# Kernel tuning notes

Measured on AMD Instinct MI355X. Metric: run time of the kernel, lower is better.

The kernel has to match this reference:

```python
import jax, jax.numpy as jnp
import numpy as np

B, IN_CAPS, IN_DIM = 64, 512, 128
NUM_CAPS, DIM_CAPS, NUM_ROUTING = 32, 32, 3


def squash(x, axis=-1):
    sn = jnp.sum(x * x, axis=axis, keepdims=True)
    return (sn / (1.0 + sn)) * x / (jnp.sqrt(sn) + 1e-8)


def setup_inputs() -> dict:
    key = jax.random.key(0)
    k1, k2, k3 = jax.random.split(key, 3)
    input_tensor = jax.random.normal(k1, (B, IN_CAPS, IN_DIM), dtype=jnp.float32)
    W = 0.001 * jax.random.normal(k2, (NUM_CAPS, IN_DIM, DIM_CAPS), dtype=jnp.float32)
    b0 = jax.random.uniform(k3, (B, NUM_CAPS, IN_CAPS, 1), dtype=jnp.float32)
    return {"input_tensor": input_tensor, "W": W, "b0": b0}


def reference(input_tensor, W, b0):
    # u_hat: (B, num_caps, in_caps, dim_caps)
    u_hat = jnp.einsum('bid,ndc->bnic', input_tensor, W)
    temp_u_hat = jax.lax.stop_gradient(u_hat)
    b = b0
    for _ in range(NUM_ROUTING - 1):
        c = jax.nn.softmax(b, axis=1)            # (B, num_caps, in_caps, 1)
        s = jnp.sum(c * temp_u_hat, axis=2)      # (B, num_caps, dim_caps)
        v = squash(s)
        uv = jnp.einsum('bnic,bnc->bni', temp_u_hat, v)[..., None]
        b = b + uv
    c = jax.nn.softmax(b, axis=1)
    s = jnp.sum(c * u_hat, axis=2)
    return squash(s)                             # (B, num_caps, dim_caps)
```

## Files before the change

kernel.cpp:

```cpp
#include <hip/hip_runtime.h>
#include <math.h>

#define Bsz 64
#define IC  512
#define KD  128
#define NC  32
#define DC  32
#define CHUNK 64
#define NCH   8
#define NBLK  512
#define NTHR  256

#define CSTR 36

#define CXP_SZ (Bsz * NCH * NC * KD)
#define WV_SZ  (Bsz * NC * KD)
#define BB_SZ  (Bsz * NC * IC)

__device__ __forceinline__ int xaddr(int i, int kq) {
    return i * KD + ((((kq) + (i >> 2)) & 31) << 2);
}

__global__ __launch_bounds__(NTHR)
void kA(const float* __restrict__ bb_in, const float* __restrict__ x_g,
        float* __restrict__ cxp)
{
    __shared__ float x_s[CHUNK * KD];
    __shared__ float bb_s[NC][CHUNK];
    __shared__ float c_sT[CHUNK * CSTR];

    const int t = threadIdx.x, blk = blockIdx.x;
    const int b = blk >> 3, ch = blk & 7, i0g = ch * CHUNK;

    for (int rep = 0; rep < 8; ++rep) {
        int v = t + rep * NTHR;
        int i = v >> 5, kq = v & 31;
        float4 val = *(const float4*)(x_g + ((size_t)(b * IC + i0g + i)) * KD + (kq << 2));
        *(float4*)(x_s + xaddr(i, kq)) = val;
    }
    for (int rep = 0; rep < 2; ++rep) {
        int v = t + rep * NTHR;
        int n = v >> 4, i4 = v & 15;
        *(float4*)(&bb_s[n][i4 << 2]) =
            *(const float4*)(bb_in + ((size_t)(b * NC + n)) * IC + i0g + (i4 << 2));
    }
    __syncthreads();

    if (t < CHUNK) {
        const int ii = t;
        float m = -1e30f;
        #pragma unroll
        for (int n = 0; n < NC; ++n) m = fmaxf(m, bb_s[n][ii]);
        float e[NC]; float sum = 0.f;
        #pragma unroll
        for (int n = 0; n < NC; ++n) { float ev = __expf(bb_s[n][ii] - m); e[n] = ev; sum += ev; }
        const float inv = 1.f / sum;
        float* crow = c_sT + ii * CSTR;
        #pragma unroll
        for (int n = 0; n < NC; ++n) crow[n] = e[n] * inv;
    }
    __syncthreads();

    const int tn = t & 7, tk = t >> 3;
    const int n0 = tn << 2;
    float4 acc0 = {0,0,0,0}, acc1 = {0,0,0,0}, acc2 = {0,0,0,0}, acc3 = {0,0,0,0};
    for (int ii = 0; ii < CHUNK; ++ii) {
        const float4 c4 = *(const float4*)(c_sT + ii * CSTR + n0);
        const float4 x4 = *(const float4*)(x_s + xaddr(ii, tk));
        acc0.x += c4.x*x4.x; acc0.y += c4.x*x4.y; acc0.z += c4.x*x4.z; acc0.w += c4.x*x4.w;
        acc1.x += c4.y*x4.x; acc1.y += c4.y*x4.y; acc1.z += c4.y*x4.z; acc1.w += c4.y*x4.w;
        acc2.x += c4.z*x4.x; acc2.y += c4.z*x4.y; acc2.z += c4.z*x4.z; acc2.w += c4.z*x4.w;
        acc3.x += c4.w*x4.x; acc3.y += c4.w*x4.y; acc3.z += c4.w*x4.z; acc3.w += c4.w*x4.w;
    }
    float* base = cxp + ((size_t)(b * NCH + ch)) * NC * KD + (tk << 2);
    *(float4*)(base + (size_t)(n0 + 0) * KD) = acc0;
    *(float4*)(base + (size_t)(n0 + 1) * KD) = acc1;
    *(float4*)(base + (size_t)(n0 + 2) * KD) = acc2;
    *(float4*)(base + (size_t)(n0 + 3) * KD) = acc3;
}

__global__ __launch_bounds__(NTHR)
void kB(const float* __restrict__ cxp, const float* __restrict__ W_g,
        float* __restrict__ wv_g, float* __restrict__ out_g, int final_)
{
    __shared__ float w_s[KD * DC];
    __shared__ float cxs[4 * KD];
    __shared__ float vs_s[4][DC];

    const int t = threadIdx.x, blk = blockIdx.x;
    const int pb_n = blk & 31, pb_b0 = (blk >> 5) * 4;

    for (int rep = 0; rep < 4; ++rep) {
        int v = t + rep * NTHR;
        *(float4*)(w_s + (v << 2)) = *(const float4*)(W_g + (size_t)pb_n * KD * DC + (v << 2));
    }
    if (t < 128) {
        const int bsub = t >> 5, k4 = t & 31;
        float4 s4 = {0,0,0,0};
        const float* p = cxp + (((size_t)(pb_b0 + bsub) * NCH) * NC + pb_n) * KD + (k4 << 2);
        #pragma unroll
        for (int c2 = 0; c2 < NCH; ++c2) {
            float4 v4 = *(const float4*)(p + (size_t)c2 * NC * KD);
            s4.x += v4.x; s4.y += v4.y; s4.z += v4.z; s4.w += v4.w;
        }
        *(float4*)(cxs + bsub * KD + (k4 << 2)) = s4;
    }
    __syncthreads();

    if (t < 128) {
        const int bsub = t >> 5, d = t & 31;
        float s = 0.f;
        const float* crow = cxs + bsub * KD;
        for (int k = 0; k < KD; ++k) s += crow[k] * w_s[k * DC + d];
        float sn = s * s;
        #pragma unroll
        for (int off = 1; off < 32; off <<= 1) sn += __shfl_xor(sn, off, 64);
        const float vv = s * (sn / ((1.f + sn) * (sqrtf(sn) + 1e-8f)));
        if (final_) {
            out_g[((size_t)(pb_b0 + bsub) * NC + pb_n) * DC + d] = vv;
        } else {
            vs_s[bsub][d] = vv;
        }
    }
    if (!final_) {
        __syncthreads();
        const int bsub = t >> 6, kk = t & 63;
        for (int k = kk; k < KD; k += 64) {
            float acc = 0.f;
            const float* wrow = w_s + k * DC;
            const float* vrow = &vs_s[bsub][0];
            #pragma unroll
            for (int d = 0; d < DC; ++d) acc += wrow[d] * vrow[d];
            wv_g[((size_t)(pb_b0 + bsub) * NC + pb_n) * KD + k] = acc;
        }
    }
}

__global__ __launch_bounds__(NTHR)
void kC(const float* __restrict__ bb_in, const float* __restrict__ x_g,
        const float* __restrict__ wv_g, float* __restrict__ bb_out)
{
    __shared__ float x_s[CHUNK * KD];
    __shared__ float bb_s[NC][CHUNK];
    __shared__ float wv_sT[KD * CSTR];

    const int t = threadIdx.x, blk = blockIdx.x;
    const int b = blk >> 3, ch = blk & 7, i0g = ch * CHUNK;

    for (int rep = 0; rep < 8; ++rep) {
        int v = t + rep * NTHR;
        int i = v >> 5, kq = v & 31;
        float4 val = *(const float4*)(x_g + ((size_t)(b * IC + i0g + i)) * KD + (kq << 2));
        *(float4*)(x_s + xaddr(i, kq)) = val;
    }
    for (int rep = 0; rep < 2; ++rep) {
        int v = t + rep * NTHR;
        int n = v >> 4, i4 = v & 15;
        *(float4*)(&bb_s[n][i4 << 2]) =
            *(const float4*)(bb_in + ((size_t)(b * NC + n)) * IC + i0g + (i4 << 2));
    }
    for (int rep = 0; rep < 4; ++rep) {
        const int n = t & 31;
        const int k4 = (t >> 5) + (rep << 3);
        float4 v4 = *(const float4*)(wv_g + ((size_t)(b * NC) + n) * KD + (k4 << 2));
        wv_sT[(k4 * 4 + 0) * CSTR + n] = v4.x;
        wv_sT[(k4 * 4 + 1) * CSTR + n] = v4.y;
        wv_sT[(k4 * 4 + 2) * CSTR + n] = v4.z;
        wv_sT[(k4 * 4 + 3) * CSTR + n] = v4.w;
    }
    __syncthreads();

    if (t < 128) {
        const int tn = t & 7, ti = t >> 3;
        const int n0 = tn << 2, i0 = ti << 2;
        float4 a0 = {0,0,0,0}, a1 = {0,0,0,0}, a2 = {0,0,0,0}, a3 = {0,0,0,0};
        for (int kq = 0; kq < 32; ++kq) {
            const float4 xr0 = *(const float4*)(x_s + xaddr(i0 + 0, kq));
            const float4 xr1 = *(const float4*)(x_s + xaddr(i0 + 1, kq));
            const float4 xr2 = *(const float4*)(x_s + xaddr(i0 + 2, kq));
            const float4 xr3 = *(const float4*)(x_s + xaddr(i0 + 3, kq));
            const float4 w0 = *(const float4*)(wv_sT + (kq * 4 + 0) * CSTR + n0);
            const float4 w1 = *(const float4*)(wv_sT + (kq * 4 + 1) * CSTR + n0);
            const float4 w2 = *(const float4*)(wv_sT + (kq * 4 + 2) * CSTR + n0);
            const float4 w3 = *(const float4*)(wv_sT + (kq * 4 + 3) * CSTR + n0);
            a0.x += xr0.x*w0.x + xr0.y*w1.x + xr0.z*w2.x + xr0.w*w3.x;
            a0.y += xr0.x*w0.y + xr0.y*w1.y + xr0.z*w2.y + xr0.w*w3.y;
            a0.z += xr0.x*w0.z + xr0.y*w1.z + xr0.z*w2.z + xr0.w*w3.z;
            a0.w += xr0.x*w0.w + xr0.y*w1.w + xr0.z*w2.w + xr0.w*w3.w;
            a1.x += xr1.x*w0.x + xr1.y*w1.x + xr1.z*w2.x + xr1.w*w3.x;
            a1.y += xr1.x*w0.y + xr1.y*w1.y + xr1.z*w2.y + xr1.w*w3.y;
            a1.z += xr1.x*w0.z + xr1.y*w1.z + xr1.z*w2.z + xr1.w*w3.z;
            a1.w += xr1.x*w0.w + xr1.y*w1.w + xr1.z*w2.w + xr1.w*w3.w;
            a2.x += xr2.x*w0.x + xr2.y*w1.x + xr2.z*w2.x + xr2.w*w3.x;
            a2.y += xr2.x*w0.y + xr2.y*w1.y + xr2.z*w2.y + xr2.w*w3.y;
            a2.z += xr2.x*w0.z + xr2.y*w1.z + xr2.z*w2.z + xr2.w*w3.z;
            a2.w += xr2.x*w0.w + xr2.y*w1.w + xr2.z*w2.w + xr2.w*w3.w;
            a3.x += xr3.x*w0.x + xr3.y*w1.x + xr3.z*w2.x + xr3.w*w3.x;
            a3.y += xr3.x*w0.y + xr3.y*w1.y + xr3.z*w2.y + xr3.w*w3.y;
            a3.z += xr3.x*w0.z + xr3.y*w1.z + xr3.z*w2.z + xr3.w*w3.z;
            a3.w += xr3.x*w0.w + xr3.y*w1.w + xr3.z*w2.w + xr3.w*w3.w;
        }
        bb_s[n0+0][i0+0] += a0.x; bb_s[n0+1][i0+0] += a0.y; bb_s[n0+2][i0+0] += a0.z; bb_s[n0+3][i0+0] += a0.w;
        bb_s[n0+0][i0+1] += a1.x; bb_s[n0+1][i0+1] += a1.y; bb_s[n0+2][i0+1] += a1.z; bb_s[n0+3][i0+1] += a1.w;
        bb_s[n0+0][i0+2] += a2.x; bb_s[n0+1][i0+2] += a2.y; bb_s[n0+2][i0+2] += a2.z; bb_s[n0+3][i0+2] += a2.w;
        bb_s[n0+0][i0+3] += a3.x; bb_s[n0+1][i0+3] += a3.y; bb_s[n0+2][i0+3] += a3.z; bb_s[n0+3][i0+3] += a3.w;
    }
    __syncthreads();

    for (int rep = 0; rep < 2; ++rep) {
        int v = t + rep * NTHR;
        int n = v >> 4, i4 = v & 15;
        *(float4*)(bb_out + ((size_t)(b * NC + n)) * IC + i0g + (i4 << 2)) =
            *(const float4*)(&bb_s[n][i4 << 2]);
    }
}

extern "C" void kernel_launch(void* const* d_in, const int* in_sizes, int n_in,
                              void* d_out, int out_size, void* d_ws, size_t ws_size,
                              hipStream_t stream) {
    const float* x  = (const float*)d_in[0];
    const float* W  = (const float*)d_in[1];
    const float* b0 = (const float*)d_in[2];
    float* out = (float*)d_out;

    float* cxp   = (float*)d_ws;
    float* wv    = cxp + CXP_SZ;
    float* bb_ws = wv + WV_SZ;

    kA<<<NBLK, NTHR, 0, stream>>>(b0, x, cxp);
    kB<<<NBLK, NTHR, 0, stream>>>(cxp, W, wv, out, 0);
    kC<<<NBLK, NTHR, 0, stream>>>(b0, x, wv, bb_ws);
    kA<<<NBLK, NTHR, 0, stream>>>(bb_ws, x, cxp);
    kB<<<NBLK, NTHR, 0, stream>>>(cxp, W, wv, out, 0);
    kC<<<NBLK, NTHR, 0, stream>>>(bb_ws, x, wv, bb_ws);
    kA<<<NBLK, NTHR, 0, stream>>>(bb_ws, x, cxp);
    kB<<<NBLK, NTHR, 0, stream>>>(cxp, W, wv, out, 1);
}
```

Measured before the change: 132.5 us.

## Fuse logit update into softmax-weighted reduction kernel and slim projection kernel

The separate kernel that updated the routing logits is merged into the kernel that computes softmax and the weighted sum over input capsules. This drops two launches and an extra read of x and the logits per routing iteration, and the last iteration no longer writes the logits back. The projection kernel now runs with 128 threads, pads the W tile to avoid bank conflicts, and computes the W·v product for four batches per thread. In exchange the fused kernel uses more shared memory per block, and its serial uv phase only uses half the threads.

```diff
diff --git a/kernel.cpp b/kernel.cpp
--- a/kernel.cpp
+++ b/kernel.cpp
@@ -10,24 +10,27 @@
 #define NCH   8
 #define NBLK  512
 #define NTHR  256
+#define NTHRB 128
 
 #define CSTR 36
+#define BSTR 68
+#define WSTR 33
 
 #define CXP_SZ (Bsz * NCH * NC * KD)
 #define WV_SZ  (Bsz * NC * KD)
-#define BB_SZ  (Bsz * NC * IC)
 
 __device__ __forceinline__ int xaddr(int i, int kq) {
     return i * KD + ((((kq) + (i >> 2)) & 31) << 2);
 }
 
 __global__ __launch_bounds__(NTHR)
-void kA(const float* __restrict__ bb_in, const float* __restrict__ x_g,
-        float* __restrict__ cxp)
+void kACX(const float* __restrict__ bb_in, const float* __restrict__ x_g,
+          const float* __restrict__ wv_g, float* __restrict__ bb_out,
+          float* __restrict__ cxp, int do_uv, int write_bb)
 {
     __shared__ float x_s[CHUNK * KD];
-    __shared__ float bb_s[NC][CHUNK];
-    __shared__ float c_sT[CHUNK * CSTR];
+    __shared__ float bb_s[NC * BSTR];
+    __shared__ float scr[KD * CSTR];
 
     const int t = threadIdx.x, blk = blockIdx.x;
     const int b = blk >> 3, ch = blk & 7, i0g = ch * CHUNK;
@@ -35,27 +38,89 @@
     for (int rep = 0; rep < 8; ++rep) {
         int v = t + rep * NTHR;
         int i = v >> 5, kq = v & 31;
-        float4 val = *(const float4*)(x_g + ((size_t)(b * IC + i0g + i)) * KD + (kq << 2));
-        *(float4*)(x_s + xaddr(i, kq)) = val;
+        *(float4*)(x_s + xaddr(i, kq)) =
+            *(const float4*)(x_g + ((size_t)(b * IC + i0g + i)) * KD + (kq << 2));
     }
     for (int rep = 0; rep < 2; ++rep) {
         int v = t + rep * NTHR;
         int n = v >> 4, i4 = v & 15;
-        *(float4*)(&bb_s[n][i4 << 2]) =
+        *(float4*)(bb_s + n * BSTR + (i4 << 2)) =
             *(const float4*)(bb_in + ((size_t)(b * NC + n)) * IC + i0g + (i4 << 2));
     }
+    if (do_uv) {
+        for (int rep = 0; rep < 4; ++rep) {
+            const int n = t & 31;
+            const int k4 = (t >> 5) + (rep << 3);
+            float4 v4 = *(const float4*)(wv_g + ((size_t)(b * NC) + n) * KD + (k4 << 2));
+            scr[(k4 * 4 + 0) * CSTR + n] = v4.x;
+            scr[(k4 * 4 + 1) * CSTR + n] = v4.y;
+            scr[(k4 * 4 + 2) * CSTR + n] = v4.z;
+            scr[(k4 * 4 + 3) * CSTR + n] = v4.w;
+        }
+    }
     __syncthreads();
+
+    if (do_uv) {
+        if (t < 128) {
+            const int tn = t & 7, ti = t >> 3;
+            const int n0 = tn << 2, i0 = ti << 2;
+            float4 a0 = {0,0,0,0}, a1 = {0,0,0,0}, a2 = {0,0,0,0}, a3 = {0,0,0,0};
+            for (int kq = 0; kq < 32; ++kq) {
+                const float4 xr0 = *(const float4*)(x_s + xaddr(i0 + 0, kq));
+                const float4 xr1 = *(const float4*)(x_s + xaddr(i0 + 1, kq));
+                const float4 xr2 = *(const float4*)(x_s + xaddr(i0 + 2, kq));
+                const float4 xr3 = *(const float4*)(x_s + xaddr(i0 + 3, kq));
+                const float4 w0 = *(const float4*)(scr + (kq * 4 + 0) * CSTR + n0);
+                const float4 w1 = *(const float4*)(scr + (kq * 4 + 1) * CSTR + n0);
+                const float4 w2 = *(const float4*)(scr + (kq * 4 + 2) * CSTR + n0);
+                const float4 w3 = *(const float4*)(scr + (kq * 4 + 3) * CSTR + n0);
+                a0.x += xr0.x*w0.x + xr0.y*w1.x + xr0.z*w2.x + xr0.w*w3.x;
+                a0.y += xr0.x*w0.y + xr0.y*w1.y + xr0.z*w2.y + xr0.w*w3.y;
+                a0.z += xr0.x*w0.z + xr0.y*w1.z + xr0.z*w2.z + xr0.w*w3.z;
+                a0.w += xr0.x*w0.w + xr0.y*w1.w + xr0.z*w2.w + xr0.w*w3.w;
+                a1.x += xr1.x*w0.x + xr1.y*w1.x + xr1.z*w2.x + xr1.w*w3.x;
+                a1.y += xr1.x*w0.y + xr1.y*w1.y + xr1.z*w2.y + xr1.w*w3.y;
+                a1.z += xr1.x*w0.z + xr1.y*w1.z + xr1.z*w2.z + xr1.w*w3.z;
+                a1.w += xr1.x*w0.w + xr1.y*w1.w + xr1.z*w2.w + xr1.w*w3.w;
+                a2.x += xr2.x*w0.x + xr2.y*w1.x + xr2.z*w2.x + xr2.w*w3.x;
+                a2.y += xr2.x*w0.y + xr2.y*w1.y + xr2.z*w2.y + xr2.w*w3.y;
+                a2.z += xr2.x*w0.z + xr2.y*w1.z + xr2.z*w2.z + xr2.w*w3.z;
+                a2.w += xr2.x*w0.w + xr2.y*w1.w + xr2.z*w2.w + xr2.w*w3.w;
+                a3.x += xr3.x*w0.x + xr3.y*w1.x + xr3.z*w2.x + xr3.w*w3.x;
+                a3.y += xr3.x*w0.y + xr3.y*w1.y + xr3.z*w2.y + xr3.w*w3.y;
+                a3.z += xr3.x*w0.z + xr3.y*w1.z + xr3.z*w2.z + xr3.w*w3.z;
+                a3.w += xr3.x*w0.w + xr3.y*w1.w + xr3.z*w2.w + xr3.w*w3.w;
+            }
+            bb_s[(n0+0)*BSTR + i0+0] += a0.x; bb_s[(n0+1)*BSTR + i0+0] += a0.y;
+            bb_s[(n0+2)*BSTR + i0+0] += a0.z; bb_s[(n0+3)*BSTR + i0+0] += a0.w;
+            bb_s[(n0+0)*BSTR + i0+1] += a1.x; bb_s[(n0+1)*BSTR + i0+1] += a1.y;
+            bb_s[(n0+2)*BSTR + i0+1] += a1.z; bb_s[(n0+3)*BSTR + i0+1] += a1.w;
+            bb_s[(n0+0)*BSTR + i0+2] += a2.x; bb_s[(n0+1)*BSTR + i0+2] += a2.y;
+            bb_s[(n0+2)*BSTR + i0+2] += a2.z; bb_s[(n0+3)*BSTR + i0+2] += a2.w;
+            bb_s[(n0+0)*BSTR + i0+3] += a3.x; bb_s[(n0+1)*BSTR + i0+3] += a3.y;
+            bb_s[(n0+2)*BSTR + i0+3] += a3.z; bb_s[(n0+3)*BSTR + i0+3] += a3.w;
+        }
+        __syncthreads();
+        if (write_bb) {
+            for (int rep = 0; rep < 2; ++rep) {
+                int v = t + rep * NTHR;
+                int n = v >> 4, i4 = v & 15;
+                *(float4*)(bb_out + ((size_t)(b * NC + n)) * IC + i0g + (i4 << 2)) =
+                    *(const float4*)(bb_s + n * BSTR + (i4 << 2));
+            }
+        }
+    }
 
     if (t < CHUNK) {
         const int ii = t;
         float m = -1e30f;
         #pragma unroll
-        for (int n = 0; n < NC; ++n) m = fmaxf(m, bb_s[n][ii]);
+        for (int n = 0; n < NC; ++n) m = fmaxf(m, bb_s[n * BSTR + ii]);
         float e[NC]; float sum = 0.f;
         #pragma unroll
-        for (int n = 0; n < NC; ++n) { float ev = __expf(bb_s[n][ii] - m); e[n] = ev; sum += ev; }
+        for (int n = 0; n < NC; ++n) { float ev = __expf(bb_s[n * BSTR + ii] - m); e[n] = ev; sum += ev; }
         const float inv = 1.f / sum;
-        float* crow = c_sT + ii * CSTR;
+        float* crow = scr + ii * CSTR;
         #pragma unroll
         for (int n = 0; n < NC; ++n) crow[n] = e[n] * inv;
     }
@@ -65,7 +130,7 @@
     const int n0 = tn << 2;
     float4 acc0 = {0,0,0,0}, acc1 = {0,0,0,0}, acc2 = {0,0,0,0}, acc3 = {0,0,0,0};
     for (int ii = 0; ii < CHUNK; ++ii) {
-        const float4 c4 = *(const float4*)(c_sT + ii * CSTR + n0);
+        const float4 c4 = *(const float4*)(scr + ii * CSTR + n0);
         const float4 x4 = *(const float4*)(x_s + xaddr(ii, tk));
         acc0.x += c4.x*x4.x; acc0.y += c4.x*x4.y; acc0.z += c4.x*x4.z; acc0.w += c4.x*x4.w;
         acc1.x += c4.y*x4.x; acc1.y += c4.y*x4.y; acc1.z += c4.y*x4.z; acc1.w += c4.y*x4.w;
@@ -79,22 +144,25 @@
     *(float4*)(base + (size_t)(n0 + 3) * KD) = acc3;
 }
 
-__global__ __launch_bounds__(NTHR)
+__global__ __launch_bounds__(NTHRB)
 void kB(const float* __restrict__ cxp, const float* __restrict__ W_g,
         float* __restrict__ wv_g, float* __restrict__ out_g, int final_)
 {
-    __shared__ float w_s[KD * DC];
+    __shared__ float w_s[KD * WSTR];
     __shared__ float cxs[4 * KD];
     __shared__ float vs_s[4][DC];
 
     const int t = threadIdx.x, blk = blockIdx.x;
     const int pb_n = blk & 31, pb_b0 = (blk >> 5) * 4;
 
-    for (int rep = 0; rep < 4; ++rep) {
-        int v = t + rep * NTHR;
-        *(float4*)(w_s + (v << 2)) = *(const float4*)(W_g + (size_t)pb_n * KD * DC + (v << 2));
-    }
-    if (t < 128) {
+    for (int rep = 0; rep < 8; ++rep) {
+        int v = t + rep * NTHRB;
+        int k = v >> 3, d0 = (v & 7) << 2;
+        float4 w4 = *(const float4*)(W_g + (size_t)pb_n * KD * DC + (v << 2));
+        float* dst = w_s + k * WSTR + d0;
+        dst[0] = w4.x; dst[1] = w4.y; dst[2] = w4.z; dst[3] = w4.w;
+    }
+    {
         const int bsub = t >> 5, k4 = t & 31;
         float4 s4 = {0,0,0,0};
         const float* p = cxp + (((size_t)(pb_b0 + bsub) * NCH) * NC + pb_n) * KD + (k4 << 2);
@@ -107,111 +175,35 @@
     }
     __syncthreads();
 
-    if (t < 128) {
-        const int bsub = t >> 5, d = t & 31;
-        float s = 0.f;
-        const float* crow = cxs + bsub * KD;
-        for (int k = 0; k < KD; ++k) s += crow[k] * w_s[k * DC + d];
-        float sn = s * s;
-        #pragma unroll
-        for (int off = 1; off < 32; off <<= 1) sn += __shfl_xor(sn, off, 64);
-        const float vv = s * (sn / ((1.f + sn) * (sqrtf(sn) + 1e-8f)));
-        if (final_) {
-            out_g[((size_t)(pb_b0 + bsub) * NC + pb_n) * DC + d] = vv;
-        } else {
-            vs_s[bsub][d] = vv;
-        }
-    }
-    if (!final_) {
+    const int bsub = t >> 5, d = t & 31;
+    float s = 0.f;
+    const float* crow = cxs + bsub * KD;
+    for (int k = 0; k < KD; ++k) s += crow[k] * w_s[k * WSTR + d];
+    float sn = s * s;
+    #pragma unroll
+    for (int off = 1; off < 32; off <<= 1) sn += __shfl_xor(sn, off, 64);
+    const float vv = s * (sn / ((1.f + sn) * (sqrtf(sn) + 1e-8f)));
+
+    if (final_) {
+        out_g[((size_t)(pb_b0 + bsub) * NC + pb_n) * DC + d] = vv;
+    } else {
+        vs_s[bsub][d] = vv;
         __syncthreads();
-        const int bsub = t >> 6, kk = t & 63;
-        for (int k = kk; k < KD; k += 64) {
-            float acc = 0.f;
-            const float* wrow = w_s + k * DC;
-            const float* vrow = &vs_s[bsub][0];
-            #pragma unroll
-            for (int d = 0; d < DC; ++d) acc += wrow[d] * vrow[d];
-            wv_g[((size_t)(pb_b0 + bsub) * NC + pb_n) * KD + k] = acc;
-        }
-    }
-}
-
-__global__ __launch_bounds__(NTHR)
-void kC(const float* __restrict__ bb_in, const float* __restrict__ x_g,
-        const float* __restrict__ wv_g, float* __restrict__ bb_out)
-{
-    __shared__ float x_s[CHUNK * KD];
-    __shared__ float bb_s[NC][CHUNK];
-    __shared__ float wv_sT[KD * CSTR];
-
-    const int t = threadIdx.x, blk = blockIdx.x;
-    const int b = blk >> 3, ch = blk & 7, i0g = ch * CHUNK;
-
-    for (int rep = 0; rep < 8; ++rep) {
-        int v = t + rep * NTHR;
-        int i = v >> 5, kq = v & 31;
-        float4 val = *(const float4*)(x_g + ((size_t)(b * IC + i0g + i)) * KD + (kq << 2));
-        *(float4*)(x_s + xaddr(i, kq)) = val;
-    }
-    for (int rep = 0; rep < 2; ++rep) {
-        int v = t + rep * NTHR;
-        int n = v >> 4, i4 = v & 15;
-        *(float4*)(&bb_s[n][i4 << 2]) =
-            *(const float4*)(bb_in + ((size_t)(b * NC + n)) * IC + i0g + (i4 << 2));
-    }
-    for (int rep = 0; rep < 4; ++rep) {
-        const int n = t & 31;
-        const int k4 = (t >> 5) + (rep << 3);
-        float4 v4 = *(const float4*)(wv_g + ((size_t)(b * NC) + n) * KD + (k4 << 2));
-        wv_sT[(k4 * 4 + 0) * CSTR + n] = v4.x;
-        wv_sT[(k4 * 4 + 1) * CSTR + n] = v4.y;
-        wv_sT[(k4 * 4 + 2) * CSTR + n] = v4.z;
-        wv_sT[(k4 * 4 + 3) * CSTR + n] = v4.w;
-    }
-    __syncthreads();
-
-    if (t < 128) {
-        const int tn = t & 7, ti = t >> 3;
-        const int n0 = tn << 2, i0 = ti << 2;
-        float4 a0 = {0,0,0,0}, a1 = {0,0,0,0}, a2 = {0,0,0,0}, a3 = {0,0,0,0};
-        for (int kq = 0; kq < 32; ++kq) {
-            const float4 xr0 = *(const float4*)(x_s + xaddr(i0 + 0, kq));
-            const float4 xr1 = *(const float4*)(x_s + xaddr(i0 + 1, kq));
-            const float4 xr2 = *(const float4*)(x_s + xaddr(i0 + 2, kq));
-            const float4 xr3 = *(const float4*)(x_s + xaddr(i0 + 3, kq));
-            const float4 w0 = *(const float4*)(wv_sT + (kq * 4 + 0) * CSTR + n0);
-            const float4 w1 = *(const float4*)(wv_sT + (kq * 4 + 1) * CSTR + n0);
-            const float4 w2 = *(const float4*)(wv_sT + (kq * 4 + 2) * CSTR + n0);
-            const float4 w3 = *(const float4*)(wv_sT + (kq * 4 + 3) * CSTR + n0);
-            a0.x += xr0.x*w0.x + xr0.y*w1.x + xr0.z*w2.x + xr0.w*w3.x;
-            a0.y += xr0.x*w0.y + xr0.y*w1.y + xr0.z*w2.y + xr0.w*w3.y;
-            a0.z += xr0.x*w0.z + xr0.y*w1.z + xr0.z*w2.z + xr0.w*w3.z;
-            a0.w += xr0.x*w0.w + xr0.y*w1.w + xr0.z*w2.w + xr0.w*w3.w;
-            a1.x += xr1.x*w0.x + xr1.y*w1.x + xr1.z*w2.x + xr1.w*w3.x;
-            a1.y += xr1.x*w0.y + xr1.y*w1.y + xr1.z*w2.y + xr1.w*w3.y;
-            a1.z += xr1.x*w0.z + xr1.y*w1.z + xr1.z*w2.z + xr1.w*w3.z;
-            a1.w += xr1.x*w0.w + xr1.y*w1.w + xr1.z*w2.w + xr1.w*w3.w;
-            a2.x += xr2.x*w0.x + xr2.y*w1.x + xr2.z*w2.x + xr2.w*w3.x;
-            a2.y += xr2.x*w0.y + xr2.y*w1.y + xr2.z*w2.y + xr2.w*w3.y;
-            a2.z += xr2.x*w0.z + xr2.y*w1.z + xr2.z*w2.z + xr2.w*w3.z;
-            a2.w += xr2.x*w0.w + xr2.y*w1.w + xr2.z*w2.w + xr2.w*w3.w;
-            a3.x += xr3.x*w0.x + xr3.y*w1.x + xr3.z*w2.x + xr3.w*w3.x;
-            a3.y += xr3.x*w0.y + xr3.y*w1.y + xr3.z*w2.y + xr3.w*w3.y;
-            a3.z += xr3.x*w0.z + xr3.y*w1.z + xr3.z*w2.z + xr3.w*w3.z;
-            a3.w += xr3.x*w0.w + xr3.y*w1.w + xr3.z*w2.w + xr3.w*w3.w;
-        }
-        bb_s[n0+0][i0+0] += a0.x; bb_s[n0+1][i0+0] += a0.y; bb_s[n0+2][i0+0] += a0.z; bb_s[n0+3][i0+0] += a0.w;
-        bb_s[n0+0][i0+1] += a1.x; bb_s[n0+1][i0+1] += a1.y; bb_s[n0+2][i0+1] += a1.z; bb_s[n0+3][i0+1] += a1.w;
-        bb_s[n0+0][i0+2] += a2.x; bb_s[n0+1][i0+2] += a2.y; bb_s[n0+2][i0+2] += a2.z; bb_s[n0+3][i0+2] += a2.w;
-        bb_s[n0+0][i0+3] += a3.x; bb_s[n0+1][i0+3] += a3.y; bb_s[n0+2][i0+3] += a3.z; bb_s[n0+3][i0+3] += a3.w;
-    }
-    __syncthreads();
-
-    for (int rep = 0; rep < 2; ++rep) {
-        int v = t + rep * NTHR;
-        int n = v >> 4, i4 = v & 15;
-        *(float4*)(bb_out + ((size_t)(b * NC + n)) * IC + i0g + (i4 << 2)) =
-            *(const float4*)(&bb_s[n][i4 << 2]);
+        const int k = t;
+        float a0 = 0.f, a1 = 0.f, a2 = 0.f, a3 = 0.f;
+        #pragma unroll
+        for (int dd = 0; dd < DC; ++dd) {
+            const float wk = w_s[k * WSTR + dd];
+            a0 += wk * vs_s[0][dd];
+            a1 += wk * vs_s[1][dd];
+            a2 += wk * vs_s[2][dd];
+            a3 += wk * vs_s[3][dd];
+        }
+        size_t base = (((size_t)pb_b0 * NC) + pb_n) * KD + k;
+        wv_g[base                      ] = a0;
+        wv_g[base + 1 * (size_t)NC * KD] = a1;
+        wv_g[base + 2 * (size_t)NC * KD] = a2;
+        wv_g[base + 3 * (size_t)NC * KD] = a3;
     }
 }
 
@@ -227,12 +219,10 @@
     float* wv    = cxp + CXP_SZ;
     float* bb_ws = wv + WV_SZ;
 
-    kA<<<NBLK, NTHR, 0, stream>>>(b0, x, cxp);
-    kB<<<NBLK, NTHR, 0, stream>>>(cxp, W, wv, out, 0);
-    kC<<<NBLK, NTHR, 0, stream>>>(b0, x, wv, bb_ws);
-    kA<<<NBLK, NTHR, 0, stream>>>(bb_ws, x, cxp);
-    kB<<<NBLK, NTHR, 0, stream>>>(cxp, W, wv, out, 0);
-    kC<<<NBLK, NTHR, 0, stream>>>(bb_ws, x, wv, bb_ws);
-    kA<<<NBLK, NTHR, 0, stream>>>(bb_ws, x, cxp);
-    kB<<<NBLK, NTHR, 0, stream>>>(cxp, W, wv, out, 1);
-}
+    kACX<<<NBLK, NTHR, 0, stream>>>(b0, x, nullptr, nullptr, cxp, 0, 0);
+    kB  <<<NBLK, NTHRB, 0, stream>>>(cxp, W, wv, out, 0);
+    kACX<<<NBLK, NTHR, 0, stream>>>(b0, x, wv, bb_ws, cxp, 1, 1);
+    kB  <<<NBLK, NTHRB, 0, stream>>>(cxp, W, wv, out, 0);
+    kACX<<<NBLK, NTHR, 0, stream>>>(bb_ws, x, wv, nullptr, cxp, 1, 0);
+    kB  <<<NBLK, NTHRB, 0, stream>>>(cxp, W, wv, out, 1);
+}
```

Measured after the change: 126.9 us. 4.2% less time.
